# Optimization experiments

Measured on AMD Instinct MI355X. Metric: run time of the kernel, lower is better.

Reference implementation:

```python
import jax, jax.numpy as jnp
import numpy as np

B, N, C = 32, 320, 768
H = 12
LT, LS = 64, 256
HD = C // H
MLP_H = 4 * C
EPS = 1e-5


def _ln(x, g, b):
    m = jnp.mean(x, axis=-1, keepdims=True)
    v = jnp.var(x, axis=-1, keepdims=True)
    return (x - m) * jax.lax.rsqrt(v + EPS) * g + b


def setup_inputs() -> dict:
    key = jax.random.key(0)
    ks = jax.random.split(key, 16)
    s = 0.02
    inp = {
        'x': jax.random.normal(ks[0], (B, N, C), jnp.float32),
        'global_index_template': jax.random.randint(ks[1], (B, LT), 0, LT),
        'global_index_search': jax.random.randint(ks[2], (B, LS), 0, LS),
        'g1': jnp.ones((C,), jnp.float32), 'b1': jnp.zeros((C,), jnp.float32),
        'Wqkv': jax.random.normal(ks[3], (C, 3 * C), jnp.float32) * s,
        'Wproj': jax.random.normal(ks[4], (C, C), jnp.float32) * s,
        'bproj': jnp.zeros((C,), jnp.float32),
        'g2': jnp.ones((C,), jnp.float32), 'b2': jnp.zeros((C,), jnp.float32),
        'W1': jax.random.normal(ks[5], (C, MLP_H), jnp.float32) * s,
        'bm1': jnp.zeros((MLP_H,), jnp.float32),
        'W2': jax.random.normal(ks[6], (MLP_H, C), jnp.float32) * s,
        'bm2': jnp.zeros((C,), jnp.float32),
        'Wg': jax.random.normal(ks[7], (C, C), jnp.float32) * s,
        'bg': jnp.zeros((C,), jnp.float32),
        'g3': jnp.ones((C,), jnp.float32), 'b3': jnp.zeros((C,), jnp.float32),
    }
    return inp


def reference(x, global_index_template, global_index_search, g1, b1, Wqkv, Wproj, bproj,
              g2, b2, W1, bm1, W2, bm2, Wg, bg, g3, b3):
    scale = HD ** (-0.5)
    # --- Attention ---
    xn = _ln(x, g1, b1)
    qkv = (xn @ Wqkv).reshape(B, N, 3, H, HD)
    q, k, v = qkv[:, :, 0], qkv[:, :, 1], qkv[:, :, 2]  # [B,N,H,HD]
    logits = jnp.einsum('bnhd,bmhd->bhnm', q, k) * scale
    attn = jax.nn.softmax(logits, axis=-1)  # [B,H,N,N]
    ctx = jnp.einsum('bhnm,bmhd->bnhd', attn, v).reshape(B, N, C)
    x = x + (ctx @ Wproj + bproj)
    # --- MLP ---
    h = jax.nn.gelu(_ln(x, g2, b2) @ W1 + bm1, approximate=False)
    x = x + (h @ W2 + bm2)
    # --- Block-adjacency from attention (avg pooling) ---
    w_ts = jnp.sum(attn[:, :, :LT, LT:], axis=1) / H  # [B,LT,LS]
    w_ts = jax.nn.softmax(w_ts, axis=2)
    adj = jnp.zeros((B, N, N), x.dtype)
    adj = adj.at[:, :LT, LT:].set(w_ts)
    adj = adj.at[:, LT:, :LT].set(jnp.swapaxes(w_ts, 1, 2))
    # --- GCN layer ---
    support = x @ Wg + bg
    x = jnp.einsum('bnm,bmc->bnc', adj, support)
    x = x + _ln(x, g3, b3)
    return x
```

## Files before the change

kernel.cpp:

```cpp
#include <hip/hip_runtime.h>
#include <stdint.h>

#define NB 32
#define NSEQ 320
#define CDIM 768
#define NH 12
#define HD 64
#define MLPH 3072
#define MROWS (NB*NSEQ)

typedef __attribute__((ext_vector_type(8))) short v8s;
typedef __attribute__((ext_vector_type(4))) float v4f;

__device__ __forceinline__ unsigned short f2b(float f){
  unsigned int u = __float_as_uint(f);
  u += 0x7fffu + ((u >> 16) & 1u);
  return (unsigned short)(u >> 16);
}
__device__ __forceinline__ float b2f(unsigned short h){
  return __uint_as_float(((unsigned int)h) << 16);
}
__device__ __forceinline__ void glds16(const unsigned short* g, unsigned short* l){
  __builtin_amdgcn_global_load_lds(
      (const __attribute__((address_space(1))) void*)g,
      (__attribute__((address_space(3))) void*)l, 16, 0, 0);
}

__global__ __launch_bounds__(256)
void castT(const float* __restrict__ W, unsigned short* __restrict__ Wt, int K, int N){
  __shared__ float tile[32][33];
  const int k0 = blockIdx.x * 32, n0 = blockIdx.y * 32;
  const int tx = threadIdx.x & 31, ty = threadIdx.x >> 5;
  #pragma unroll
  for (int i = 0; i < 32; i += 8)
    tile[ty + i][tx] = W[(size_t)(k0 + ty + i) * N + n0 + tx];
  __syncthreads();
  #pragma unroll
  for (int i = 0; i < 32; i += 8)
    Wt[(size_t)(n0 + ty + i) * K + k0 + tx] = f2b(tile[tx][ty + i]);
}

__global__ __launch_bounds__(192)
void ln_to_bf16(const float* __restrict__ x, const float* __restrict__ g,
                const float* __restrict__ be, unsigned short* __restrict__ out){
  const int row = blockIdx.x;
  const int t = threadIdx.x, w = t >> 6, l = t & 63;
  const float4 v = *(const float4*)(x + (size_t)row * CDIM + t * 4);
  float s  = v.x + v.y + v.z + v.w;
  float s2 = v.x*v.x + v.y*v.y + v.z*v.z + v.w*v.w;
  __shared__ float r1[3], r2[3];
  #pragma unroll
  for (int d = 1; d < 64; d <<= 1){ s += __shfl_xor(s, d, 64); s2 += __shfl_xor(s2, d, 64); }
  if (l == 0){ r1[w] = s; r2[w] = s2; }
  __syncthreads();
  const float S = r1[0] + r1[1] + r1[2];
  const float S2 = r2[0] + r2[1] + r2[2];
  const float mean = S * (1.0f / CDIM);
  const float var  = S2 * (1.0f / CDIM) - mean * mean;
  const float rs = rsqrtf(var + 1e-5f);
  const float4 gg = *(const float4*)(g + t * 4);
  const float4 bb = *(const float4*)(be + t * 4);
  ushort4 o;
  o.x = f2b((v.x - mean) * rs * gg.x + bb.x);
  o.y = f2b((v.y - mean) * rs * gg.y + bb.y);
  o.z = f2b((v.z - mean) * rs * gg.z + bb.z);
  o.w = f2b((v.w - mean) * rs * gg.w + bb.w);
  *(ushort4*)(out + (size_t)row * CDIM + t * 4) = o;
}

template<bool BIAS, bool RES, bool GELU, bool WB, bool WF>
__global__ __launch_bounds__(256, 2)
void gemm_bt(const unsigned short* __restrict__ A, const unsigned short* __restrict__ Bt,
             int M, int N, int K,
             const float* __restrict__ bias, const float* __restrict__ res,
             unsigned short* __restrict__ outb, float* __restrict__ outf){
  __shared__ __align__(16) unsigned short As[128 * 32];
  __shared__ __align__(16) unsigned short Bs[128 * 32];
  const int t = threadIdx.x;
  const int w = t >> 6, l = t & 63;
  const int bm = blockIdx.x, bn = blockIdx.y;
  const int wr = w >> 1, wc = w & 1;
  v4f acc[4][4] = {};

  const int srow = (w << 5) + (l >> 2);
  const int sseg = (l & 3) * 8;
  const unsigned short* Ag = A + (size_t)(bm * 128 + srow) * K + sseg;
  const unsigned short* Bg = Bt + (size_t)(bn * 128 + srow) * K + sseg;
  unsigned short* Al = As + (w * 32) * 32;
  unsigned short* Bl = Bs + (w * 32) * 32;

  const int ksteps = K >> 5;
  for (int ks = 0; ks < ksteps; ++ks){
    const int k0 = ks << 5;
    if (ks) __syncthreads();
    glds16(Ag + k0, Al);
    glds16(Ag + (size_t)16 * K + k0, Al + 16 * 32);
    glds16(Bg + k0, Bl);
    glds16(Bg + (size_t)16 * K + k0, Bl + 16 * 32);
    __syncthreads();
    const int kk = (l >> 4) << 3;
    v8s af[4], bfr[4];
    #pragma unroll
    for (int mi = 0; mi < 4; ++mi)
      af[mi] = *(const v8s*)&As[(wr * 64 + mi * 16 + (l & 15)) * 32 + kk];
    #pragma unroll
    for (int ni = 0; ni < 4; ++ni)
      bfr[ni] = *(const v8s*)&Bs[(wc * 64 + ni * 16 + (l & 15)) * 32 + kk];
    #pragma unroll
    for (int mi = 0; mi < 4; ++mi)
      #pragma unroll
      for (int ni = 0; ni < 4; ++ni)
        acc[mi][ni] = __builtin_amdgcn_mfma_f32_16x16x32_bf16(af[mi], bfr[ni], acc[mi][ni], 0, 0, 0);
  }

  const int r0 = bm * 128 + wr * 64 + ((l >> 4) << 2);
  const int c0 = bn * 128 + wc * 64 + (l & 15);
  #pragma unroll
  for (int mi = 0; mi < 4; ++mi){
    #pragma unroll
    for (int rr = 0; rr < 4; ++rr){
      const int row = r0 + mi * 16 + rr;
      #pragma unroll
      for (int ni = 0; ni < 4; ++ni){
        const int col = c0 + ni * 16;
        float c = acc[mi][ni][rr];
        if (BIAS) c += bias[col];
        if (RES)  c += res[(size_t)row * N + col];
        if (GELU) c = 0.5f * c * (1.0f + erff(c * 0.70710678118f));
        if (WB) outb[(size_t)row * N + col] = f2b(c);
        if (WF) outf[(size_t)row * N + col] = c;
      }
    }
  }
}

__global__ __launch_bounds__(256, 2)
void attn_kernel(const unsigned short* __restrict__ qkv,
                 unsigned short* __restrict__ ctx,
                 float* __restrict__ wparts){
  __shared__ __align__(16) unsigned short Qs[64 * 72];
  __shared__ __align__(16) unsigned short KV[64 * 72];
  __shared__ __align__(16) unsigned short Ps[64 * 328];
  const int t = threadIdx.x;
  const int w = t >> 6, l = t & 63;
  const int bid = blockIdx.x;
  const int qt = bid % 5;
  const int h  = (bid / 5) % NH;
  const int b  = bid / (5 * NH);
  const size_t base = (size_t)b * NSEQ * 2304 + h * 64;

  {
    const int r = t >> 3, seg = t & 7;
    #pragma unroll
    for (int i = 0; i < 2; ++i){
      const int r2 = r + 32 * i;
      const unsigned short* src = qkv + base + (size_t)(qt * 64 + r2) * 2304 + seg * 8;
      *(uint4*)&Qs[r2 * 72 + seg * 8] = *(const uint4*)src;
    }
  }
  __syncthreads();
  const int qr = 16 * w + (l & 15);
  const v8s aq0 = *(const v8s*)&Qs[qr * 72 + ((l >> 4) << 3)];
  const v8s aq1 = *(const v8s*)&Qs[qr * 72 + 32 + ((l >> 4) << 3)];

  v4f sacc[20] = {};
  for (int kt = 0; kt < 5; ++kt){
    __syncthreads();
    {
      const int r = t >> 3, seg = t & 7;
      #pragma unroll
      for (int i = 0; i < 2; ++i){
        const int r2 = r + 32 * i;
        const unsigned short* src = qkv + base + 768 + (size_t)(kt * 64 + r2) * 2304 + seg * 8;
        *(uint4*)&KV[r2 * 72 + seg * 8] = *(const uint4*)src;
      }
    }
    __syncthreads();
    #pragma unroll
    for (int f = 0; f < 4; ++f){
      const int kr = 16 * f + (l & 15);
      const v8s b0 = *(const v8s*)&KV[kr * 72 + ((l >> 4) << 3)];
      const v8s b1 = *(const v8s*)&KV[kr * 72 + 32 + ((l >> 4) << 3)];
      sacc[kt * 4 + f] = __builtin_amdgcn_mfma_f32_16x16x32_bf16(aq0, b0, sacc[kt * 4 + f], 0, 0, 0);
      sacc[kt * 4 + f] = __builtin_amdgcn_mfma_f32_16x16x32_bf16(aq1, b1, sacc[kt * 4 + f], 0, 0, 0);
    }
  }

  const float scale = 0.125f;
  #pragma unroll
  for (int r = 0; r < 4; ++r){
    float m = -1e30f;
    #pragma unroll
    for (int f = 0; f < 20; ++f) m = fmaxf(m, sacc[f][r]);
    #pragma unroll
    for (int d = 1; d < 16; d <<= 1) m = fmaxf(m, __shfl_xor(m, d, 64));
    const float Ms = m * scale;
    float sum = 0.f;
    #pragma unroll
    for (int f = 0; f < 20; ++f){ float p = expf(sacc[f][r] * scale - Ms); sacc[f][r] = p; sum += p; }
    #pragma unroll
    for (int d = 1; d < 16; d <<= 1) sum += __shfl_xor(sum, d, 64);
    const float inv = 1.0f / sum;
    const int rowq = 16 * w + ((l >> 4) << 2) + r;
    #pragma unroll
    for (int f = 0; f < 20; ++f)
      Ps[rowq * 328 + f * 16 + (l & 15)] = f2b(sacc[f][r] * inv);
    if (qt == 0){
      #pragma unroll
      for (int f = 4; f < 20; ++f)
        wparts[(((size_t)b * NH + h) * 64 + rowq) * 256 + (f - 4) * 16 + (l & 15)] = sacc[f][r] * inv;
    }
  }

  v4f cacc[4] = {};
  for (int kt = 0; kt < 5; ++kt){
    __syncthreads();
    {
      const int m = t & 31, d0 = (t >> 5) * 8;
      #pragma unroll
      for (int i = 0; i < 2; ++i){
        const int m2 = m + 32 * i;
        const unsigned short* src = qkv + base + 1536 + (size_t)(kt * 64 + m2) * 2304 + d0;
        uint4 dv = *(const uint4*)src;
        const unsigned short* e = (const unsigned short*)&dv;
        #pragma unroll
        for (int jj = 0; jj < 8; ++jj) KV[(d0 + jj) * 72 + m2] = e[jj];
      }
    }
    __syncthreads();
    const int pr = 16 * w + (l & 15);
    const v8s pa0 = *(const v8s*)&Ps[pr * 328 + kt * 64 + ((l >> 4) << 3)];
    const v8s pa1 = *(const v8s*)&Ps[pr * 328 + kt * 64 + 32 + ((l >> 4) << 3)];
    #pragma unroll
    for (int f = 0; f < 4; ++f){
      const int vc = 16 * f + (l & 15);
      const v8s bv0 = *(const v8s*)&KV[vc * 72 + ((l >> 4) << 3)];
      const v8s bv1 = *(const v8s*)&KV[vc * 72 + 32 + ((l >> 4) << 3)];
      cacc[f] = __builtin_amdgcn_mfma_f32_16x16x32_bf16(pa0, bv0, cacc[f], 0, 0, 0);
      cacc[f] = __builtin_amdgcn_mfma_f32_16x16x32_bf16(pa1, bv1, cacc[f], 0, 0, 0);
    }
  }
  #pragma unroll
  for (int f = 0; f < 4; ++f)
    #pragma unroll
    for (int rr = 0; rr < 4; ++rr){
      const int rowq = 16 * w + ((l >> 4) << 2) + rr;
      const int col = 16 * f + (l & 15);
      ctx[(size_t)(b * NSEQ + qt * 64 + rowq) * CDIM + h * 64 + col] = f2b(cacc[f][rr]);
    }
}

__global__ __launch_bounds__(256)
void wts_softmax(const float* __restrict__ wparts,
                 unsigned short* __restrict__ wtsb,
                 unsigned short* __restrict__ wtsbT){
  const int row = blockIdx.x;
  const int b = row >> 6, n = row & 63;
  const int j = threadIdx.x;
  const int w = j >> 6, l = j & 63;
  float s = 0.f;
  #pragma unroll
  for (int hh = 0; hh < NH; ++hh)
    s += wparts[(((size_t)b * NH + hh) * 64 + n) * 256 + j];
  s *= (1.0f / NH);
  __shared__ float red[8];
  float m = s;
  #pragma unroll
  for (int d = 1; d < 64; d <<= 1) m = fmaxf(m, __shfl_xor(m, d, 64));
  if (l == 0) red[w] = m;
  __syncthreads();
  m = fmaxf(fmaxf(red[0], red[1]), fmaxf(red[2], red[3]));
  const float e = expf(s - m);
  float sm = e;
  #pragma unroll
  for (int d = 1; d < 64; d <<= 1) sm += __shfl_xor(sm, d, 64);
  if (l == 0) red[4 + w] = sm;
  __syncthreads();
  const float tot = red[4] + red[5] + red[6] + red[7];
  const unsigned short p = f2b(e / tot);
  wtsb [((size_t)b * 64 + n) * 256 + j] = p;
  wtsbT[((size_t)b * 256 + j) * 64 + n] = p;
}

__global__ __launch_bounds__(256)
void transT(const unsigned short* __restrict__ in, unsigned short* __restrict__ out){
  __shared__ unsigned short tile[64][65];
  const int c0 = blockIdx.x * 64, n0 = blockIdx.y * 64, b = blockIdx.z;
  const int tx = threadIdx.x & 31, ty = threadIdx.x >> 5;
  const unsigned short* ib = in + (size_t)b * NSEQ * CDIM;
  unsigned short* ob = out + (size_t)b * CDIM * NSEQ;
  #pragma unroll
  for (int i = 0; i < 64; i += 8){
    const unsigned int v = *(const unsigned int*)&ib[(size_t)(n0 + ty + i) * CDIM + c0 + tx * 2];
    tile[tx * 2][ty + i]     = (unsigned short)(v & 0xffff);
    tile[tx * 2 + 1][ty + i] = (unsigned short)(v >> 16);
  }
  __syncthreads();
  #pragma unroll
  for (int i = 0; i < 64; i += 8){
    const int c = ty + i;
    const unsigned int v = (unsigned int)tile[c][tx * 2] | ((unsigned int)tile[c][tx * 2 + 1] << 16);
    *(unsigned int*)&ob[(size_t)(c0 + c) * NSEQ + n0 + tx * 2] = v;
  }
}

template<int KC, int SH2>
__global__ __launch_bounds__(256, 2)
void graph_gemm(const unsigned short* __restrict__ A, int KTOT,
                const unsigned short* __restrict__ supT, int koff,
                float* __restrict__ y, int rowoff){
  __shared__ __align__(16) unsigned short As[64 * KC];
  __shared__ __align__(16) unsigned short Bs[128 * KC];
  const int t = threadIdx.x, w = t >> 6, l = t & 63;
  const int mt = blockIdx.x, ct = blockIdx.y, b = blockIdx.z;
  const char* Ab = (const char*)(A + (size_t)b * 16384 + (size_t)mt * 64 * KTOT);
  const char* Bb = (const char*)(supT + (size_t)b * CDIM * NSEQ);
  v4f acc[4][2] = {};

  const int nch = KTOT / KC;
  for (int ch = 0; ch < nch; ++ch){
    if (ch) __syncthreads();
    const int kbase = (koff + ch * KC) * 2;
    #pragma unroll
    for (int i = 0; i < KC / 32; ++i){
      const int gi = w * (KC / 32) + i;
      const int X = gi * 1024 + l * 16;
      const int c = X >> SH2;
      const int k2 = (X & (KC * 2 - 1)) ^ ((c & 7) << 4);
      glds16((const unsigned short*)(Ab + (size_t)c * (KTOT * 2) + ch * KC * 2 + k2),
             As + (gi * 512));
    }
    #pragma unroll
    for (int i = 0; i < KC / 16; ++i){
      const int gi = w * (KC / 16) + i;
      const int X = gi * 1024 + l * 16;
      const int c = X >> SH2;
      const int k2 = (X & (KC * 2 - 1)) ^ ((c & 7) << 4);
      glds16((const unsigned short*)(Bb + (size_t)(ct * 128 + c) * (NSEQ * 2) + kbase + k2),
             Bs + (gi * 512));
    }
    __syncthreads();
    #pragma unroll
    for (int ks = 0; ks < KC / 32; ++ks){
      const int kbyte = ks * 64 + ((l >> 4) << 4);
      v8s af[4], bf2[2];
      #pragma unroll
      for (int mi = 0; mi < 4; ++mi){
        const int r = mi * 16 + (l & 15);
        af[mi] = *(const v8s*)((const char*)As + (r << SH2) + (kbyte ^ ((r & 7) << 4)));
      }
      #pragma unroll
      for (int ni = 0; ni < 2; ++ni){
        const int rb = w * 32 + ni * 16 + (l & 15);
        bf2[ni] = *(const v8s*)((const char*)Bs + (rb << SH2) + (kbyte ^ ((rb & 7) << 4)));
      }
      #pragma unroll
      for (int mi = 0; mi < 4; ++mi)
        #pragma unroll
        for (int ni = 0; ni < 2; ++ni)
          acc[mi][ni] = __builtin_amdgcn_mfma_f32_16x16x32_bf16(af[mi], bf2[ni], acc[mi][ni], 0, 0, 0);
    }
  }

  const int r0 = rowoff + mt * 64 + ((l >> 4) << 2);
  const int c0 = ct * 128 + w * 32 + (l & 15);
  #pragma unroll
  for (int mi = 0; mi < 4; ++mi)
    #pragma unroll
    for (int ni = 0; ni < 2; ++ni)
      #pragma unroll
      for (int rr = 0; rr < 4; ++rr)
        y[((size_t)b * NSEQ + r0 + mi * 16 + rr) * CDIM + c0 + ni * 16] = acc[mi][ni][rr];
}

__global__ __launch_bounds__(192)
void ln_final(const float* __restrict__ y, const float* __restrict__ g3,
              const float* __restrict__ b3, float* __restrict__ out){
  const int row = blockIdx.x;
  const int t = threadIdx.x, w = t >> 6, l = t & 63;
  const float4 v = *(const float4*)(y + (size_t)row * CDIM + t * 4);
  float s  = v.x + v.y + v.z + v.w;
  float s2 = v.x*v.x + v.y*v.y + v.z*v.z + v.w*v.w;
  __shared__ float r1[3], r2[3];
  #pragma unroll
  for (int d = 1; d < 64; d <<= 1){ s += __shfl_xor(s, d, 64); s2 += __shfl_xor(s2, d, 64); }
  if (l == 0){ r1[w] = s; r2[w] = s2; }
  __syncthreads();
  const float S = r1[0] + r1[1] + r1[2];
  const float S2 = r2[0] + r2[1] + r2[2];
  const float mean = S * (1.0f / CDIM);
  const float var  = S2 * (1.0f / CDIM) - mean * mean;
  const float rs = rsqrtf(var + 1e-5f);
  const float4 gg = *(const float4*)(g3 + t * 4);
  const float4 bb = *(const float4*)(b3 + t * 4);
  float4 o;
  o.x = v.x + (v.x - mean) * rs * gg.x + bb.x;
  o.y = v.y + (v.y - mean) * rs * gg.y + bb.y;
  o.z = v.z + (v.z - mean) * rs * gg.z + bb.z;
  o.w = v.w + (v.w - mean) * rs * gg.w + bb.w;
  *(float4*)(out + (size_t)row * CDIM + t * 4) = o;
}

extern "C" void kernel_launch(void* const* d_in, const int* in_sizes, int n_in,
                              void* d_out, int out_size, void* d_ws, size_t ws_size,
                              hipStream_t stream){
  (void)in_sizes; (void)n_in; (void)out_size; (void)ws_size;
  const float* x    = (const float*)d_in[0];
  const float* g1   = (const float*)d_in[3];
  const float* b1   = (const float*)d_in[4];
  const float* Wqkv = (const float*)d_in[5];
  const float* Wproj= (const float*)d_in[6];
  const float* bproj= (const float*)d_in[7];
  const float* g2   = (const float*)d_in[8];
  const float* b2   = (const float*)d_in[9];
  const float* W1   = (const float*)d_in[10];
  const float* bm1  = (const float*)d_in[11];
  const float* W2   = (const float*)d_in[12];
  const float* bm2  = (const float*)d_in[13];
  const float* Wg   = (const float*)d_in[14];
  const float* bg   = (const float*)d_in[15];
  const float* g3   = (const float*)d_in[16];
  const float* b3   = (const float*)d_in[17];
  float* out = (float*)d_out;
  char* ws = (char*)d_ws;

  unsigned short* wqkvT = (unsigned short*)(ws + 0);
  unsigned short* wprojT= (unsigned short*)(ws + 3538944);
  unsigned short* w1T   = (unsigned short*)(ws + 4718592);
  unsigned short* w2T   = (unsigned short*)(ws + 9437184);
  unsigned short* wgT   = (unsigned short*)(ws + 14155776);
  unsigned short* xn1   = (unsigned short*)(ws + 15335424);
  unsigned short* qkvb  = (unsigned short*)(ws + 31064064);
  unsigned short* hb    = (unsigned short*)(ws + 15335424);
  unsigned short* supT  = (unsigned short*)(ws + 15335424);
  unsigned short* ctxb  = (unsigned short*)(ws + 78249984);
  unsigned short* x2b   = (unsigned short*)(ws + 78249984);
  unsigned short* xn2   = (unsigned short*)(ws + 93978624);
  unsigned short* supb  = (unsigned short*)(ws + 93978624);
  float*          x1    = (float*)(ws + 109707264);
  float*          wparts= (float*)(ws + 109707264);
  float*          yb    = (float*)(ws + 109707264);
  unsigned short* wtsb  = (unsigned short*)(ws + 141164544);
  unsigned short* wtsbT = (unsigned short*)(ws + 142213120);

  castT<<<dim3(CDIM/32, 2304/32), 256, 0, stream>>>(Wqkv, wqkvT, CDIM, 2304);
  castT<<<dim3(CDIM/32, CDIM/32), 256, 0, stream>>>(Wproj, wprojT, CDIM, CDIM);
  castT<<<dim3(CDIM/32, MLPH/32), 256, 0, stream>>>(W1, w1T, CDIM, MLPH);
  castT<<<dim3(MLPH/32, CDIM/32), 256, 0, stream>>>(W2, w2T, MLPH, CDIM);
  castT<<<dim3(CDIM/32, CDIM/32), 256, 0, stream>>>(Wg, wgT, CDIM, CDIM);

  ln_to_bf16<<<MROWS, 192, 0, stream>>>(x, g1, b1, xn1);

  gemm_bt<false,false,false,true,false><<<dim3(80, 18), 256, 0, stream>>>(
      xn1, wqkvT, MROWS, 2304, CDIM, nullptr, nullptr, qkvb, nullptr);

  attn_kernel<<<NB * NH * 5, 256, 0, stream>>>(qkvb, ctxb, wparts);

  wts_softmax<<<NB * 64, 256, 0, stream>>>(wparts, wtsb, wtsbT);

  gemm_bt<true,true,false,false,true><<<dim3(80, 6), 256, 0, stream>>>(
      ctxb, wprojT, MROWS, CDIM, CDIM, bproj, x, nullptr, x1);

  ln_to_bf16<<<MROWS, 192, 0, stream>>>(x1, g2, b2, xn2);

  gemm_bt<true,false,true,true,false><<<dim3(80, 24), 256, 0, stream>>>(
      xn2, w1T, MROWS, MLPH, CDIM, bm1, nullptr, hb, nullptr);

  gemm_bt<true,true,false,true,false><<<dim3(80, 6), 256, 0, stream>>>(
      hb, w2T, MROWS, CDIM, MLPH, bm2, x1, x2b, nullptr);

  gemm_bt<true,false,false,true,false><<<dim3(80, 6), 256, 0, stream>>>(
      x2b, wgT, MROWS, CDIM, CDIM, bg, nullptr, supb, nullptr);

  transT<<<dim3(CDIM/64, NSEQ/64, NB), 256, 0, stream>>>(supb, supT);

  graph_gemm<128, 8><<<dim3(1, 6, NB), 256, 0, stream>>>(wtsb, 256, supT, 64, yb, 0);
  graph_gemm<64, 7><<<dim3(4, 6, NB), 256, 0, stream>>>(wtsbT, 64, supT, 0, yb, 64);

  ln_final<<<MROWS, 192, 0, stream>>>(yb, g3, b3, out);
}
```

Measured before the change: 502.0 us.

## Replace GEMM with 8-wave double-buffered swizzled-LDS pipelined kernel

Replaces the simple 128x128, single-buffered bf16 MFMA GEMM with a 512-thread kernel using 256-row tiles, a K-step of 64, double-buffered LDS with XOR swizzling, and interleaved async global-to-LDS loads between MFMA quadrants, using s_setprio and explicit vmcnt waits. The goal is to hide global memory latency, cut LDS bank conflicts and raise per-block data reuse across all five linear layers. It adds register pressure from the larger accumulator array and depends on exact vmcnt counting. Larger tiles also produce fewer blocks, for example 240 blocks for the N=768 GEMMs.

```diff
diff --git a/kernel.cpp b/kernel.cpp
--- a/kernel.cpp
+++ b/kernel.cpp
@@ -68,62 +68,131 @@
   *(ushort4*)(out + (size_t)row * CDIM + t * 4) = o;
 }
 
-template<bool BIAS, bool RES, bool GELU, bool WB, bool WF>
-__global__ __launch_bounds__(256, 2)
-void gemm_bt(const unsigned short* __restrict__ A, const unsigned short* __restrict__ Bt,
-             int M, int N, int K,
-             const float* __restrict__ bias, const float* __restrict__ res,
-             unsigned short* __restrict__ outb, float* __restrict__ outf){
-  __shared__ __align__(16) unsigned short As[128 * 32];
-  __shared__ __align__(16) unsigned short Bs[128 * 32];
-  const int t = threadIdx.x;
-  const int w = t >> 6, l = t & 63;
+#define BARX() do { asm volatile("" ::: "memory"); __builtin_amdgcn_s_barrier(); asm volatile("" ::: "memory"); } while(0)
+
+#define READA(BUF, MH) do { \
+  _Pragma("unroll") \
+  for (int mi = 0; mi < 4; ++mi){ \
+    const int row_ = wm*128 + (MH)*64 + mi*16 + (l & 15); \
+    _Pragma("unroll") \
+    for (int kk = 0; kk < 2; ++kk) \
+      af[mi][kk] = *(const v8s*)((const char*)(BUF) + row_*128 + ((kk*64 + ((l>>4)<<4)) ^ ((l&7)<<4))); \
+  } } while(0)
+
+#define READB(BUF, NH, BR) do { \
+  _Pragma("unroll") \
+  for (int nf = 0; nf < NHF; ++nf){ \
+    const int row_ = wn*(NF*16) + (NH)*(NHF*16) + nf*16 + (l & 15); \
+    _Pragma("unroll") \
+    for (int kk = 0; kk < 2; ++kk) \
+      BR[nf][kk] = *(const v8s*)((const char*)(BUF) + row_*128 + ((kk*64 + ((l>>4)<<4)) ^ ((l&7)<<4))); \
+  } } while(0)
+
+#define QUADX(MH, NH, BR) do { \
+  __builtin_amdgcn_s_setprio(1); \
+  _Pragma("unroll") \
+  for (int mi = 0; mi < 4; ++mi) \
+    _Pragma("unroll") \
+    for (int nf = 0; nf < NHF; ++nf){ \
+      v4f c_ = acc[(MH)*4+mi][(NH)*NHF+nf]; \
+      c_ = __builtin_amdgcn_mfma_f32_16x16x32_bf16(af[mi][0], BR[nf][0], c_, 0, 0, 0); \
+      c_ = __builtin_amdgcn_mfma_f32_16x16x32_bf16(af[mi][1], BR[nf][1], c_, 0, 0, 0); \
+      acc[(MH)*4+mi][(NH)*NHF+nf] = c_; \
+    } \
+  __builtin_amdgcn_s_setprio(0); \
+} while(0)
+
+template<int NF, bool BIAS, bool RES, bool GELU, bool WB, bool WF>
+__global__ __launch_bounds__(512, 2)
+void gemm8p(const unsigned short* __restrict__ A, const unsigned short* __restrict__ Bt,
+            int N, int K,
+            const float* __restrict__ bias, const float* __restrict__ res,
+            unsigned short* __restrict__ outb, float* __restrict__ outf){
+  constexpr int BN  = NF * 64;
+  constexpr int NHF = NF / 2;
+  __shared__ __align__(16) unsigned short lds[2*256*64 + 2*BN*64];
+  unsigned short* const A0 = lds;
+  unsigned short* const A1 = lds + 256*64;
+  unsigned short* const B0 = lds + 2*256*64;
+  unsigned short* const B1 = lds + 2*256*64 + BN*64;
+
+  const int tid = threadIdx.x;
+  const int w = tid >> 6, l = tid & 63;
+  const int wm = w >> 2, wn = w & 3;
   const int bm = blockIdx.x, bn = blockIdx.y;
-  const int wr = w >> 1, wc = w & 1;
-  v4f acc[4][4] = {};
-
-  const int srow = (w << 5) + (l >> 2);
-  const int sseg = (l & 3) * 8;
-  const unsigned short* Ag = A + (size_t)(bm * 128 + srow) * K + sseg;
-  const unsigned short* Bg = Bt + (size_t)(bn * 128 + srow) * K + sseg;
-  unsigned short* Al = As + (w * 32) * 32;
-  unsigned short* Bl = Bs + (w * 32) * 32;
-
-  const int ksteps = K >> 5;
-  for (int ks = 0; ks < ksteps; ++ks){
-    const int k0 = ks << 5;
-    if (ks) __syncthreads();
-    glds16(Ag + k0, Al);
-    glds16(Ag + (size_t)16 * K + k0, Al + 16 * 32);
-    glds16(Bg + k0, Bl);
-    glds16(Bg + (size_t)16 * K + k0, Bl + 16 * 32);
-    __syncthreads();
-    const int kk = (l >> 4) << 3;
-    v8s af[4], bfr[4];
-    #pragma unroll
-    for (int mi = 0; mi < 4; ++mi)
-      af[mi] = *(const v8s*)&As[(wr * 64 + mi * 16 + (l & 15)) * 32 + kk];
-    #pragma unroll
-    for (int ni = 0; ni < 4; ++ni)
-      bfr[ni] = *(const v8s*)&Bs[(wc * 64 + ni * 16 + (l & 15)) * 32 + kk];
-    #pragma unroll
-    for (int mi = 0; mi < 4; ++mi)
-      #pragma unroll
-      for (int ni = 0; ni < 4; ++ni)
-        acc[mi][ni] = __builtin_amdgcn_mfma_f32_16x16x32_bf16(af[mi], bfr[ni], acc[mi][ni], 0, 0, 0);
-  }
-
-  const int r0 = bm * 128 + wr * 64 + ((l >> 4) << 2);
-  const int c0 = bn * 128 + wc * 64 + (l & 15);
-  #pragma unroll
-  for (int mi = 0; mi < 4; ++mi){
+  const int nt = K >> 6;
+
+  const int swz = ((l & 7) ^ (l >> 3)) << 3;
+  const int lr8 = l >> 3;
+
+  v4f acc[8][NF];
+  #pragma unroll
+  for (int i = 0; i < 8; ++i)
+    #pragma unroll
+    for (int j = 0; j < NF; ++j) acc[i][j] = v4f{0.f, 0.f, 0.f, 0.f};
+
+  v8s af[4][2], b0r[NHF][2], b1r[NHF][2];
+
+  auto stageA = [&](unsigned short* buf, int h, int kt){
+    #pragma unroll
+    for (int i = 0; i < 2; ++i){
+      const int lr = i*128 + h*64 + w*8;
+      glds16(A + (size_t)(bm*256 + lr + lr8) * K + kt*64 + swz, buf + lr*64);
+    }
+  };
+  auto stageB = [&](unsigned short* buf, int nh, int kt){
+    if constexpr (NF == 4){
+      #pragma unroll
+      for (int i = 0; i < 2; ++i){
+        const int lr = (i*2 + (w>>2))*64 + nh*32 + (w&3)*8;
+        glds16(Bt + (size_t)(bn*BN + lr + lr8) * K + kt*64 + swz, buf + lr*64);
+      }
+    } else {
+      const int lr = (w>>1)*32 + nh*16 + (w&1)*8;
+      glds16(Bt + (size_t)(bn*BN + lr + lr8) * K + kt*64 + swz, buf + lr*64);
+    }
+  };
+
+  stageA(A0, 0, 0); stageB(B0, 0, 0); stageB(B0, 1, 0); stageA(A0, 1, 0);
+  stageA(A1, 0, 1); stageB(B1, 0, 1); stageB(B1, 1, 1); stageA(A1, 1, 1);
+  if constexpr (NF == 4) asm volatile("s_waitcnt vmcnt(8)" ::: "memory");
+  else                   asm volatile("s_waitcnt vmcnt(6)" ::: "memory");
+  __builtin_amdgcn_s_barrier();
+
+  #pragma unroll 1
+  for (int t = 0; t < nt; ++t){
+    unsigned short* const Ac = (t & 1) ? A1 : A0;
+    unsigned short* const Bc = (t & 1) ? B1 : B0;
+    READA(Ac, 0); READB(Bc, 0, b0r);
+    BARX(); QUADX(0, 0, b0r); BARX();
+    READB(Bc, 1, b1r);
+    if (t + 2 < nt) stageA(Ac, 0, t + 2);
+    BARX(); QUADX(0, 1, b1r); BARX();
+    READA(Ac, 1);
+    if (t + 2 < nt) stageB(Bc, 0, t + 2);
+    BARX(); QUADX(1, 1, b1r); BARX();
+    if (t + 2 < nt){
+      stageB(Bc, 1, t + 2); stageA(Ac, 1, t + 2);
+      if constexpr (NF == 4) asm volatile("s_waitcnt vmcnt(8)" ::: "memory");
+      else                   asm volatile("s_waitcnt vmcnt(6)" ::: "memory");
+    } else {
+      asm volatile("s_waitcnt vmcnt(0)" ::: "memory");
+    }
+    BARX(); QUADX(1, 0, b0r); BARX();
+  }
+
+  const int r0 = bm*256 + wm*128 + ((l >> 4) << 2);
+  const int c0 = bn*BN + wn*(NF*16) + (l & 15);
+  #pragma unroll
+  for (int mg = 0; mg < 8; ++mg){
+    const int rowoff = (mg >> 2)*64 + (mg & 3)*16;
     #pragma unroll
     for (int rr = 0; rr < 4; ++rr){
-      const int row = r0 + mi * 16 + rr;
-      #pragma unroll
-      for (int ni = 0; ni < 4; ++ni){
-        const int col = c0 + ni * 16;
-        float c = acc[mi][ni][rr];
+      const int row = r0 + rowoff + rr;
+      #pragma unroll
+      for (int ng = 0; ng < NF; ++ng){
+        const int col = c0 + ng*16;
+        float c = acc[mg][ng][rr];
         if (BIAS) c += bias[col];
         if (RES)  c += res[(size_t)row * N + col];
         if (GELU) c = 0.5f * c * (1.0f + erff(c * 0.70710678118f));
@@ -133,6 +202,9 @@
     }
   }
 }
+#undef READA
+#undef READB
+#undef QUADX
 
 __global__ __launch_bounds__(256, 2)
 void attn_kernel(const unsigned short* __restrict__ qkv,
@@ -451,26 +523,26 @@
 
   ln_to_bf16<<<MROWS, 192, 0, stream>>>(x, g1, b1, xn1);
 
-  gemm_bt<false,false,false,true,false><<<dim3(80, 18), 256, 0, stream>>>(
-      xn1, wqkvT, MROWS, 2304, CDIM, nullptr, nullptr, qkvb, nullptr);
+  gemm8p<2,false,false,false,true,false><<<dim3(40, 18), 512, 0, stream>>>(
+      xn1, wqkvT, 2304, CDIM, nullptr, nullptr, qkvb, nullptr);
 
   attn_kernel<<<NB * NH * 5, 256, 0, stream>>>(qkvb, ctxb, wparts);
 
   wts_softmax<<<NB * 64, 256, 0, stream>>>(wparts, wtsb, wtsbT);
 
-  gemm_bt<true,true,false,false,true><<<dim3(80, 6), 256, 0, stream>>>(
-      ctxb, wprojT, MROWS, CDIM, CDIM, bproj, x, nullptr, x1);
+  gemm8p<2,true,true,false,false,true><<<dim3(40, 6), 512, 0, stream>>>(
+      ctxb, wprojT, CDIM, CDIM, bproj, x, nullptr, x1);
 
   ln_to_bf16<<<MROWS, 192, 0, stream>>>(x1, g2, b2, xn2);
 
-  gemm_bt<true,false,true,true,false><<<dim3(80, 24), 256, 0, stream>>>(
-      xn2, w1T, MROWS, MLPH, CDIM, bm1, nullptr, hb, nullptr);
-
-  gemm_bt<true,true,false,true,false><<<dim3(80, 6), 256, 0, stream>>>(
-      hb, w2T, MROWS, CDIM, MLPH, bm2, x1, x2b, nullptr);
-
-  gemm_bt<true,false,false,true,false><<<dim3(80, 6), 256, 0, stream>>>(
-      x2b, wgT, MROWS, CDIM, CDIM, bg, nullptr, supb, nullptr);
+  gemm8p<4,true,false,true,true,false><<<dim3(40, 12), 512, 0, stream>>>(
+      xn2, w1T, MLPH, CDIM, bm1, nullptr, hb, nullptr);
+
+  gemm8p<2,true,true,false,true,false><<<dim3(40, 6), 512, 0, stream>>>(
+      hb, w2T, CDIM, MLPH, bm2, x1, x2b, nullptr);
+
+  gemm8p<2,true,false,false,true,false><<<dim3(40, 6), 512, 0, stream>>>(
+      x2b, wgT, CDIM, CDIM, bg, nullptr, supb, nullptr);
 
   transT<<<dim3(CDIM/64, NSEQ/64, NB), 256, 0, stream>>>(supb, supT);
 
```

Result: slower. 620.7 us (+23.7%).

## Use 64-wide K tiles with XOR-swizzled LDS in GEMMs and fuse weight casts

Applied to the files above, without the earlier changes.

The GEMM kernel now stages 64-element K slices per tile instead of 32, which halves the number of barrier-separated load rounds. It applies an XOR swizzle to the LDS layout so fragment reads avoid bank conflicts. The five separate weight cast-transpose launches are merged into one kernel that dispatches on block index, saving launch overhead. LDS use per block doubles, which may reduce occupancy, and there is still no double buffering.

```diff
diff --git a/kernel.cpp b/kernel.cpp
--- a/kernel.cpp
+++ b/kernel.cpp
@@ -27,9 +27,21 @@
 }
 
 __global__ __launch_bounds__(256)
-void castT(const float* __restrict__ W, unsigned short* __restrict__ Wt, int K, int N){
+void castAll(const float* __restrict__ Wqkv, const float* __restrict__ Wproj,
+             const float* __restrict__ W1,   const float* __restrict__ W2,
+             const float* __restrict__ Wg,
+             unsigned short* __restrict__ wqkvT, unsigned short* __restrict__ wprojT,
+             unsigned short* __restrict__ w1T,   unsigned short* __restrict__ w2T,
+             unsigned short* __restrict__ wgT){
+  int bid = blockIdx.x;
+  const float* W; unsigned short* Wt; int K, N, KT;
+  if (bid < 1728){ W = Wqkv; Wt = wqkvT; K = 768; N = 2304; KT = 24; }
+  else if (bid < 1728+576){ bid -= 1728; W = Wproj; Wt = wprojT; K = 768; N = 768; KT = 24; }
+  else if (bid < 1728+576+2304){ bid -= 1728+576; W = W1; Wt = w1T; K = 768; N = 3072; KT = 24; }
+  else if (bid < 1728+576+2304+2304){ bid -= 1728+576+2304; W = W2; Wt = w2T; K = 3072; N = 768; KT = 96; }
+  else { bid -= 1728+576+2304+2304; W = Wg; Wt = wgT; K = 768; N = 768; KT = 24; }
+  const int k0 = (bid % KT) * 32, n0 = (bid / KT) * 32;
   __shared__ float tile[32][33];
-  const int k0 = blockIdx.x * 32, n0 = blockIdx.y * 32;
   const int tx = threadIdx.x & 31, ty = threadIdx.x >> 5;
   #pragma unroll
   for (int i = 0; i < 32; i += 8)
@@ -70,47 +82,55 @@
 
 template<bool BIAS, bool RES, bool GELU, bool WB, bool WF>
 __global__ __launch_bounds__(256, 2)
-void gemm_bt(const unsigned short* __restrict__ A, const unsigned short* __restrict__ Bt,
-             int M, int N, int K,
-             const float* __restrict__ bias, const float* __restrict__ res,
-             unsigned short* __restrict__ outb, float* __restrict__ outf){
-  __shared__ __align__(16) unsigned short As[128 * 32];
-  __shared__ __align__(16) unsigned short Bs[128 * 32];
+void gemm_bt64(const unsigned short* __restrict__ A, const unsigned short* __restrict__ Bt,
+               int N, int K,
+               const float* __restrict__ bias, const float* __restrict__ res,
+               unsigned short* __restrict__ outb, float* __restrict__ outf){
+  __shared__ __align__(16) unsigned short As[128 * 64];
+  __shared__ __align__(16) unsigned short Bs[128 * 64];
   const int t = threadIdx.x;
   const int w = t >> 6, l = t & 63;
   const int bm = blockIdx.x, bn = blockIdx.y;
   const int wr = w >> 1, wc = w & 1;
   v4f acc[4][4] = {};
 
-  const int srow = (w << 5) + (l >> 2);
-  const int sseg = (l & 3) * 8;
-  const unsigned short* Ag = A + (size_t)(bm * 128 + srow) * K + sseg;
-  const unsigned short* Bg = Bt + (size_t)(bn * 128 + srow) * K + sseg;
-  unsigned short* Al = As + (w * 32) * 32;
-  unsigned short* Bl = Bs + (w * 32) * 32;
-
-  const int ksteps = K >> 5;
-  for (int ks = 0; ks < ksteps; ++ks){
-    const int k0 = ks << 5;
-    if (ks) __syncthreads();
-    glds16(Ag + k0, Al);
-    glds16(Ag + (size_t)16 * K + k0, Al + 16 * 32);
-    glds16(Bg + k0, Bl);
-    glds16(Bg + (size_t)16 * K + k0, Bl + 16 * 32);
-    __syncthreads();
-    const int kk = (l >> 4) << 3;
-    v8s af[4], bfr[4];
-    #pragma unroll
-    for (int mi = 0; mi < 4; ++mi)
-      af[mi] = *(const v8s*)&As[(wr * 64 + mi * 16 + (l & 15)) * 32 + kk];
-    #pragma unroll
-    for (int ni = 0; ni < 4; ++ni)
-      bfr[ni] = *(const v8s*)&Bs[(wc * 64 + ni * 16 + (l & 15)) * 32 + kk];
-    #pragma unroll
-    for (int mi = 0; mi < 4; ++mi)
-      #pragma unroll
-      for (int ni = 0; ni < 4; ++ni)
-        acc[mi][ni] = __builtin_amdgcn_mfma_f32_16x16x32_bf16(af[mi], bfr[ni], acc[mi][ni], 0, 0, 0);
+  const int srow = w * 32 + (l >> 3);
+  const int scol = ((l & 7) ^ (l >> 3)) * 8;
+  const unsigned short* Ag = A + (size_t)(bm * 128 + srow) * K + scol;
+  const unsigned short* Bg = Bt + (size_t)(bn * 128 + srow) * K + scol;
+  unsigned short* Al = As + (w * 32) * 64;
+  unsigned short* Bl = Bs + (w * 32) * 64;
+
+  const int nkt = K >> 6;
+  for (int kt = 0; kt < nkt; ++kt){
+    const int k0 = kt << 6;
+    if (kt) __syncthreads();
+    #pragma unroll
+    for (int i = 0; i < 4; ++i){
+      glds16(Ag + (size_t)(i * 8) * K + k0, Al + i * 8 * 64);
+      glds16(Bg + (size_t)(i * 8) * K + k0, Bl + i * 8 * 64);
+    }
+    __syncthreads();
+    #pragma unroll
+    for (int ks = 0; ks < 2; ++ks){
+      const int kb = ks * 64 + ((l >> 4) << 4);
+      v8s af[4], bfr[4];
+      #pragma unroll
+      for (int mi = 0; mi < 4; ++mi){
+        const int r = wr * 64 + mi * 16 + (l & 15);
+        af[mi] = *(const v8s*)((const char*)As + r * 128 + (kb ^ ((r & 7) << 4)));
+      }
+      #pragma unroll
+      for (int ni = 0; ni < 4; ++ni){
+        const int r = wc * 64 + ni * 16 + (l & 15);
+        bfr[ni] = *(const v8s*)((const char*)Bs + r * 128 + (kb ^ ((r & 7) << 4)));
+      }
+      #pragma unroll
+      for (int mi = 0; mi < 4; ++mi)
+        #pragma unroll
+        for (int ni = 0; ni < 4; ++ni)
+          acc[mi][ni] = __builtin_amdgcn_mfma_f32_16x16x32_bf16(af[mi], bfr[ni], acc[mi][ni], 0, 0, 0);
+    }
   }
 
   const int r0 = bm * 128 + wr * 64 + ((l >> 4) << 2);
@@ -443,34 +463,31 @@
   unsigned short* wtsb  = (unsigned short*)(ws + 141164544);
   unsigned short* wtsbT = (unsigned short*)(ws + 142213120);
 
-  castT<<<dim3(CDIM/32, 2304/32), 256, 0, stream>>>(Wqkv, wqkvT, CDIM, 2304);
-  castT<<<dim3(CDIM/32, CDIM/32), 256, 0, stream>>>(Wproj, wprojT, CDIM, CDIM);
-  castT<<<dim3(CDIM/32, MLPH/32), 256, 0, stream>>>(W1, w1T, CDIM, MLPH);
-  castT<<<dim3(MLPH/32, CDIM/32), 256, 0, stream>>>(W2, w2T, MLPH, CDIM);
-  castT<<<dim3(CDIM/32, CDIM/32), 256, 0, stream>>>(Wg, wgT, CDIM, CDIM);
+  castAll<<<7488, 256, 0, stream>>>(Wqkv, Wproj, W1, W2, Wg,
+                                    wqkvT, wprojT, w1T, w2T, wgT);
 
   ln_to_bf16<<<MROWS, 192, 0, stream>>>(x, g1, b1, xn1);
 
-  gemm_bt<false,false,false,true,false><<<dim3(80, 18), 256, 0, stream>>>(
-      xn1, wqkvT, MROWS, 2304, CDIM, nullptr, nullptr, qkvb, nullptr);
+  gemm_bt64<false,false,false,true,false><<<dim3(80, 18), 256, 0, stream>>>(
+      xn1, wqkvT, 2304, CDIM, nullptr, nullptr, qkvb, nullptr);
 
   attn_kernel<<<NB * NH * 5, 256, 0, stream>>>(qkvb, ctxb, wparts);
 
   wts_softmax<<<NB * 64, 256, 0, stream>>>(wparts, wtsb, wtsbT);
 
-  gemm_bt<true,true,false,false,true><<<dim3(80, 6), 256, 0, stream>>>(
-      ctxb, wprojT, MROWS, CDIM, CDIM, bproj, x, nullptr, x1);
+  gemm_bt64<true,true,false,false,true><<<dim3(80, 6), 256, 0, stream>>>(
+      ctxb, wprojT, CDIM, CDIM, bproj, x, nullptr, x1);
 
   ln_to_bf16<<<MROWS, 192, 0, stream>>>(x1, g2, b2, xn2);
 
-  gemm_bt<true,false,true,true,false><<<dim3(80, 24), 256, 0, stream>>>(
-      xn2, w1T, MROWS, MLPH, CDIM, bm1, nullptr, hb, nullptr);
-
-  gemm_bt<true,true,false,true,false><<<dim3(80, 6), 256, 0, stream>>>(
-      hb, w2T, MROWS, CDIM, MLPH, bm2, x1, x2b, nullptr);
-
-  gemm_bt<true,false,false,true,false><<<dim3(80, 6), 256, 0, stream>>>(
-      x2b, wgT, MROWS, CDIM, CDIM, bg, nullptr, supb, nullptr);
+  gemm_bt64<true,false,true,true,false><<<dim3(80, 24), 256, 0, stream>>>(
+      xn2, w1T, MLPH, CDIM, bm1, nullptr, hb, nullptr);
+
+  gemm_bt64<true,true,false,true,false><<<dim3(80, 6), 256, 0, stream>>>(
+      hb, w2T, CDIM, MLPH, bm2, x1, x2b, nullptr);
+
+  gemm_bt64<true,false,false,true,false><<<dim3(80, 6), 256, 0, stream>>>(
+      x2b, wgT, CDIM, CDIM, bg, nullptr, supb, nullptr);
 
   transT<<<dim3(CDIM/64, NSEQ/64, NB), 256, 0, stream>>>(supb, supT);
 
```

Measured after the change: 477.4 us. 1.05x faster.
